# Kernel tuning notes

Hardware: AMD Instinct MI355X
Metric: run time of the kernel (lower is better)

## Reference

```python
import jax, jax.numpy as jnp
import numpy as np

N_NODES = 100000
N_EDGES = 3200000
IN_DIM = 256
OUT_DIM = 256


def setup_inputs() -> dict:
    key = jax.random.key(0)
    k1, k2, k3, k4, k5 = jax.random.split(key, 5)
    x = jax.random.normal(k1, (N_NODES, IN_DIM), dtype=jnp.float32)
    edge_src = jax.random.randint(k2, (N_EDGES,), 0, N_NODES, dtype=jnp.int32)
    edge_dst = jax.random.randint(k3, (N_EDGES,), 0, N_NODES, dtype=jnp.int32)
    # normalized adjacency values (e.g. D^-1/2 A D^-1/2 entries)
    edge_val = jax.random.uniform(k4, (N_EDGES,), dtype=jnp.float32)
    # parameters: uniform(0,1) weight, constant 0.3 bias (matches torch init)
    weight = jax.random.uniform(k5, (IN_DIM, OUT_DIM), dtype=jnp.float32)
    bias = jnp.full((OUT_DIM,), 0.3, dtype=jnp.float32)
    return {"x": x, "edge_src": edge_src, "edge_dst": edge_dst,
            "edge_val": edge_val, "weight": weight, "bias": bias}


def reference(x, edge_src, edge_dst, edge_val, weight, bias):
    # dense feature transform: [N, in] @ [in, out] -> [N, out]
    h = x @ weight
    # sparse adjacency aggregation: out[d] = sum_e val[e] * h[src[e]] for dst[e]==d
    msgs = edge_val[:, None] * h[edge_src]              # [E, out]
    agg = jax.ops.segment_sum(msgs, edge_dst, num_segments=N_NODES)
    return agg + bias
```

## Files before the change

### kernel.cpp

```cpp
#include <hip/hip_runtime.h>

#define FDIM 256
#define BSH 6
#define NBMAX 1600
#define CH 4096
#define NSLOT 7
#define CAPB 2432
#define EPT 10

typedef __attribute__((ext_vector_type(4))) float f32x4;
typedef __attribute__((ext_vector_type(8))) short bf16x8;
typedef unsigned long long u64;

static __device__ __forceinline__ unsigned short f32_to_bf16_rtn(float f) {
    unsigned u = __builtin_bit_cast(unsigned, f);
    u += 0x7FFFu + ((u >> 16) & 1u);
    return (unsigned short)(u >> 16);
}
static __device__ __forceinline__ float bf16_to_f32(unsigned short s) {
    unsigned u = ((unsigned)s) << 16;
    return __builtin_bit_cast(float, u);
}

__global__ __launch_bounds__(256) void convert_bin_kernel(
    const float* __restrict__ x, unsigned short* __restrict__ xh, long n8,
    const float* __restrict__ W, unsigned short* __restrict__ wfrag,
    const int* __restrict__ src, const int* __restrict__ dst, const float* __restrict__ val,
    int* __restrict__ cursors, u64* __restrict__ binned, int n_edges, int nb, int bin_blocks) {
    __shared__ int hist[NBMAX];
    __shared__ int gbase[NBMAX];
    __shared__ int sbase[NBMAX];
    __shared__ int scan_s[256];
    __shared__ u64 stage[CH];
    __shared__ unsigned short bos[CH];

    const int t = threadIdx.x;

    if (blockIdx.x < 32) {
        int tt = blockIdx.x * 256 + t;
        int lane = tt & 63;
        int kt   = (tt >> 6) & 7;
        int nt   = tt >> 9;
        int col  = nt * 16 + (lane & 15);
        int k0   = kt * 32 + 8 * (lane >> 4);
        ushort4 o0, o1;
        o0.x = f32_to_bf16_rtn(W[(k0 + 0) * FDIM + col]);
        o0.y = f32_to_bf16_rtn(W[(k0 + 1) * FDIM + col]);
        o0.z = f32_to_bf16_rtn(W[(k0 + 2) * FDIM + col]);
        o0.w = f32_to_bf16_rtn(W[(k0 + 3) * FDIM + col]);
        o1.x = f32_to_bf16_rtn(W[(k0 + 4) * FDIM + col]);
        o1.y = f32_to_bf16_rtn(W[(k0 + 5) * FDIM + col]);
        o1.z = f32_to_bf16_rtn(W[(k0 + 6) * FDIM + col]);
        o1.w = f32_to_bf16_rtn(W[(k0 + 7) * FDIM + col]);
        ((ushort4*)(wfrag + (size_t)tt * 8))[0] = o0;
        ((ushort4*)(wfrag + (size_t)tt * 8))[1] = o1;
    }

    if (blockIdx.x < bin_blocks) {
        const int chunk0 = blockIdx.x * CH;
        const int m = min(CH, n_edges - chunk0);

        for (int b = t; b < nb; b += 256) hist[b] = 0;
        __syncthreads();
        for (int i = t; i < m; i += 256) atomicAdd(&hist[dst[chunk0 + i] >> BSH], 1);
        __syncthreads();
        for (int b = t; b < nb; b += 256) {
            int c = hist[b];
            gbase[b] = c ? atomicAdd(&cursors[b], c) : 0;
        }
        int loc[NSLOT]; int sum = 0;
        #pragma unroll
        for (int k = 0; k < NSLOT; ++k) {
            int b = t * NSLOT + k;
            int c = (b < nb) ? hist[b] : 0;
            loc[k] = sum; sum += c;
        }
        scan_s[t] = sum;
        __syncthreads();
        #pragma unroll
        for (int off = 1; off < 256; off <<= 1) {
            int u = (t >= off) ? scan_s[t - off] : 0;
            __syncthreads();
            scan_s[t] += u;
            __syncthreads();
        }
        int excl = scan_s[t] - sum;
        #pragma unroll
        for (int k = 0; k < NSLOT; ++k) {
            int b = t * NSLOT + k;
            if (b < nb) sbase[b] = excl + loc[k];
        }
        __syncthreads();
        for (int b = t; b < nb; b += 256) hist[b] = 0;
        __syncthreads();
        for (int i = t; i < m; i += 256) {
            int d = dst[chunk0 + i];
            int b = d >> BSH;
            int p = atomicAdd(&hist[b], 1);
            int slot = sbase[b] + p;
            unsigned w0 = (unsigned)src[chunk0 + i] | ((unsigned)(d & 63) << 17);
            unsigned w1 = __builtin_bit_cast(unsigned, val[chunk0 + i]);
            stage[slot] = (u64)w0 | ((u64)w1 << 32);
            bos[slot]   = (unsigned short)b;
        }
        __syncthreads();
        for (int i = t; i < m; i += 256) {
            int b = bos[i];
            int p = gbase[b] + (i - sbase[b]);
            if (p < CAPB)
                binned[(size_t)b * CAPB + p] = stage[i];
        }
    }

    long i = (long)blockIdx.x * 256 + t;
    long stride = (long)gridDim.x * 256;
    for (long p = i; p < n8; p += stride) {
        const float4* q = (const float4*)(x + p * 8);
        float4 a = q[0], b = q[1];
        ushort4 o0, o1;
        o0.x = f32_to_bf16_rtn(a.x); o0.y = f32_to_bf16_rtn(a.y);
        o0.z = f32_to_bf16_rtn(a.z); o0.w = f32_to_bf16_rtn(a.w);
        o1.x = f32_to_bf16_rtn(b.x); o1.y = f32_to_bf16_rtn(b.y);
        o1.z = f32_to_bf16_rtn(b.z); o1.w = f32_to_bf16_rtn(b.w);
        ((ushort4*)(xh + p * 8))[0] = o0;
        ((ushort4*)(xh + p * 8))[1] = o1;
    }
}

__global__ __launch_bounds__(256) void gather_kernel(
    const unsigned short* __restrict__ xh, const int* __restrict__ cursors,
    const u64* __restrict__ binned,
    float* __restrict__ aggf, unsigned short* __restrict__ aggb, int use_bf16, int n_nodes) {
    __shared__ u64 s2[CAPB];
    __shared__ int cnt[64], startv[64], cur[64];

    const int t = threadIdx.x, b = blockIdx.x;
    const size_t base = (size_t)b * CAPB;
    int m = cursors[b];
    if (m > CAPB) m = CAPB;

    if (t < 64) cnt[t] = 0;
    __syncthreads();
    u64 ereg[EPT];
    int nmine = 0;
    #pragma unroll
    for (int k = 0; k < EPT; ++k) {
        int i = t + k * 256;
        if (i < m) {
            u64 e = binned[base + i];
            ereg[k] = e;
            nmine = k + 1;
            atomicAdd(&cnt[(int)((e >> 17) & 63)], 1);
        }
    }
    __syncthreads();
    if (t < 64) startv[t] = cnt[t];
    __syncthreads();
    #pragma unroll
    for (int off = 1; off < 64; off <<= 1) {
        int u = 0;
        if (t < 64 && t >= off) u = startv[t - off];
        __syncthreads();
        if (t < 64) startv[t] += u;
        __syncthreads();
    }
    if (t < 64) cur[t] = startv[t] - cnt[t];
    __syncthreads();
    #pragma unroll
    for (int k = 0; k < EPT; ++k) {
        if (k < nmine) {
            u64 e = ereg[k];
            int p = atomicAdd(&cur[(int)((e >> 17) & 63)], 1);
            s2[p] = e;
        }
    }
    __syncthreads();

    const int wv = t >> 6, lane = t & 63;
    const int half = lane >> 5, l32 = lane & 31;
    for (int q = 0; q < 16; ++q) {
        const int lo = wv * 16 + q;
        const int node = (b << BSH) + lo;
        const int beg = startv[lo] - cnt[lo];
        const int end = startv[lo];
        float acc[8] = {0.f, 0.f, 0.f, 0.f, 0.f, 0.f, 0.f, 0.f};
        int j = beg;
        for (; j + 16 <= end; j += 16) {
            #pragma unroll
            for (int k = 0; k < 8; ++k) {
                u64 e = s2[j + 2 * k + half];
                float v = __builtin_bit_cast(float, (unsigned)(e >> 32));
                bf16x8 r = *(const bf16x8*)(xh + (((size_t)((unsigned)e & 0x1FFFF)) << 8) + (l32 << 3));
                #pragma unroll
                for (int d = 0; d < 8; ++d)
                    acc[d] += v * bf16_to_f32((unsigned short)r[d]);
            }
        }
        for (; j + 8 <= end; j += 8) {
            #pragma unroll
            for (int k = 0; k < 4; ++k) {
                u64 e = s2[j + 2 * k + half];
                float v = __builtin_bit_cast(float, (unsigned)(e >> 32));
                bf16x8 r = *(const bf16x8*)(xh + (((size_t)((unsigned)e & 0x1FFFF)) << 8) + (l32 << 3));
                #pragma unroll
                for (int d = 0; d < 8; ++d)
                    acc[d] += v * bf16_to_f32((unsigned short)r[d]);
            }
        }
        for (; j < end; j += 2) {
            int idx = j + half;
            u64 e = s2[idx < end ? idx : j];
            float v = (idx < end) ? __builtin_bit_cast(float, (unsigned)(e >> 32)) : 0.f;
            bf16x8 r = *(const bf16x8*)(xh + (((size_t)((unsigned)e & 0x1FFFF)) << 8) + (l32 << 3));
            #pragma unroll
            for (int d = 0; d < 8; ++d)
                acc[d] += v * bf16_to_f32((unsigned short)r[d]);
        }
        #pragma unroll
        for (int d = 0; d < 8; ++d) acc[d] += __shfl_xor(acc[d], 32);
        if (node < n_nodes) {
            float c0 = acc[4 * half + 0], c1 = acc[4 * half + 1];
            float c2 = acc[4 * half + 2], c3 = acc[4 * half + 3];
            if (use_bf16) {
                u64 w = (u64)f32_to_bf16_rtn(c0) | ((u64)f32_to_bf16_rtn(c1) << 16)
                      | ((u64)f32_to_bf16_rtn(c2) << 32) | ((u64)f32_to_bf16_rtn(c3) << 48);
                __builtin_nontemporal_store(w,
                    (u64*)(aggb + ((size_t)node << 8) + (l32 << 3) + (half << 2)));
            } else {
                f32x4 o = {c0, c1, c2, c3};
                __builtin_nontemporal_store(o,
                    (f32x4*)(aggf + ((size_t)node << 8) + (l32 << 3) + (half << 2)));
            }
        }
    }
}

template <bool BF16A>
__global__ __launch_bounds__(256) void gemm_mfma_kernel(
    const void* __restrict__ Araw, const unsigned short* __restrict__ wfrag,
    const float* __restrict__ bias, float* __restrict__ out, int n_rows) {
    int wave = (int)((blockIdx.x * 256u + threadIdx.x) >> 6);
    int lane = threadIdx.x & 63;
    int m0 = wave * 32;
    if (m0 >= n_rows) return;

    f32x4 acc[2][16];
    #pragma unroll
    for (int s = 0; s < 2; ++s)
        #pragma unroll
        for (int i = 0; i < 16; ++i) acc[s][i] = (f32x4)(0.f);

    const int arow0 = m0 + (lane & 15);
    const int arow1 = arow0 + 16;
    const int kbase = 8 * (lane >> 4);

    #pragma unroll
    for (int kt = 0; kt < 8; ++kt) {
        bf16x8 af0, af1;
        if (BF16A) {
            const unsigned short* Ab = (const unsigned short*)Araw;
            af0 = __builtin_nontemporal_load(
                (const bf16x8*)(Ab + (size_t)arow0 * FDIM + kt * 32 + kbase));
            af1 = __builtin_nontemporal_load(
                (const bf16x8*)(Ab + (size_t)arow1 * FDIM + kt * 32 + kbase));
        } else {
            const float* A = (const float*)Araw;
            const f32x4* ap0 = (const f32x4*)(A + (size_t)arow0 * FDIM + kt * 32 + kbase);
            const f32x4* ap1 = (const f32x4*)(A + (size_t)arow1 * FDIM + kt * 32 + kbase);
            f32x4 a0 = __builtin_nontemporal_load(ap0);
            f32x4 a1 = __builtin_nontemporal_load(ap0 + 1);
            f32x4 b0 = __builtin_nontemporal_load(ap1);
            f32x4 b1 = __builtin_nontemporal_load(ap1 + 1);
            #pragma unroll
            for (int j = 0; j < 4; ++j) {
                af0[j]     = (short)f32_to_bf16_rtn(a0[j]);
                af0[j + 4] = (short)f32_to_bf16_rtn(a1[j]);
                af1[j]     = (short)f32_to_bf16_rtn(b0[j]);
                af1[j + 4] = (short)f32_to_bf16_rtn(b1[j]);
            }
        }
        #pragma unroll
        for (int nt = 0; nt < 16; ++nt) {
            bf16x8 bfr = *(const bf16x8*)(wfrag + ((size_t)(nt * 8 + kt) * 64 + lane) * 8);
            acc[0][nt] = __builtin_amdgcn_mfma_f32_16x16x32_bf16(af0, bfr, acc[0][nt], 0, 0, 0);
            acc[1][nt] = __builtin_amdgcn_mfma_f32_16x16x32_bf16(af1, bfr, acc[1][nt], 0, 0, 0);
        }
    }

    const int col = lane & 15;
    #pragma unroll
    for (int s = 0; s < 2; ++s) {
        const int rbase = m0 + s * 16 + 4 * (lane >> 4);
        #pragma unroll
        for (int nt = 0; nt < 16; ++nt) {
            float bv = bias[nt * 16 + col];
            #pragma unroll
            for (int r = 0; r < 4; ++r) {
                int row = rbase + r;
                if (row < n_rows)
                    __builtin_nontemporal_store(acc[s][nt][r] + bv,
                        &out[(size_t)row * FDIM + nt * 16 + col]);
            }
        }
    }
}

extern "C" void kernel_launch(void* const* d_in, const int* in_sizes, int n_in,
                              void* d_out, int out_size, void* d_ws, size_t ws_size,
                              hipStream_t stream) {
    const float* x    = (const float*)d_in[0];
    const int*   src  = (const int*)  d_in[1];
    const int*   dst  = (const int*)  d_in[2];
    const float* val  = (const float*)d_in[3];
    const float* W    = (const float*)d_in[4];
    const float* bias = (const float*)d_in[5];
    float* out = (float*)d_out;

    int n_nodes = in_sizes[0] / FDIM;
    int n_edges = in_sizes[1];
    int nb = (n_nodes + 63) >> BSH;

    int* cursors = (int*)d_ws;
    size_t ioff = ((size_t)nb + 1) & ~(size_t)1;
    u64* binned = (u64*)((int*)d_ws + ioff);
    unsigned short* xh    = (unsigned short*)(binned + (size_t)nb * CAPB);
    unsigned short* wfrag = xh + (size_t)n_nodes * FDIM;
    unsigned short* aggb  = wfrag + 16 * 8 * 64 * 8;

    size_t need = (size_t)((char*)(aggb + (size_t)n_nodes * FDIM) - (char*)d_ws);
    int use_bf16_agg = (ws_size >= need) ? 1 : 0;

    (void)hipMemsetAsync(cursors, 0, (size_t)nb * sizeof(int), stream);

    long n8 = (long)n_nodes * FDIM / 8;
    int bin_blocks = (n_edges + CH - 1) / CH;
    convert_bin_kernel<<<2048, 256, 0, stream>>>(x, xh, n8, W, wfrag,
                                                 src, dst, val, cursors, binned,
                                                 n_edges, nb, bin_blocks);

    gather_kernel<<<nb, 256, 0, stream>>>(xh, cursors, binned,
                                          out, aggb, use_bf16_agg, n_nodes);

    int waves = (n_nodes + 31) / 32;
    int gemm_blocks = (waves + 3) / 4;
    if (use_bf16_agg)
        gemm_mfma_kernel<true><<<gemm_blocks, 256, 0, stream>>>((const void*)aggb, wfrag, bias, out, n_nodes);
    else
        gemm_mfma_kernel<false><<<gemm_blocks, 256, 0, stream>>>((const void*)out, wfrag, bias, out, n_nodes);
}
```

Before: 492.5 us.

## Reorder to transform-then-aggregate, fusing x conversion into GEMM and bias into gather

Computes h = x@W first in a bf16 MFMA GEMM that reads fp32 x directly, stores h as bf16, then gathers over h and adds bias when writing the final output. This removes the separate x-to-bf16 conversion pass and the intermediate aggregated buffer round trip. The cost is that binning no longer overlaps with x conversion, and h is now rounded to bf16 before aggregation.

```diff
diff --git a/kernel.cpp b/kernel.cpp
--- a/kernel.cpp
+++ b/kernel.cpp
@@ -22,11 +22,10 @@
     return __builtin_bit_cast(float, u);
 }
 
-__global__ __launch_bounds__(256) void convert_bin_kernel(
-    const float* __restrict__ x, unsigned short* __restrict__ xh, long n8,
-    const float* __restrict__ W, unsigned short* __restrict__ wfrag,
+__global__ __launch_bounds__(256) void bin_kernel(
     const int* __restrict__ src, const int* __restrict__ dst, const float* __restrict__ val,
-    int* __restrict__ cursors, u64* __restrict__ binned, int n_edges, int nb, int bin_blocks) {
+    int* __restrict__ cursors, u64* __restrict__ binned, int n_edges, int nb,
+    const float* __restrict__ W, unsigned short* __restrict__ wfrag) {
     __shared__ int hist[NBMAX];
     __shared__ int gbase[NBMAX];
     __shared__ int sbase[NBMAX];
@@ -56,81 +55,125 @@
         ((ushort4*)(wfrag + (size_t)tt * 8))[1] = o1;
     }
 
-    if (blockIdx.x < bin_blocks) {
-        const int chunk0 = blockIdx.x * CH;
-        const int m = min(CH, n_edges - chunk0);
-
-        for (int b = t; b < nb; b += 256) hist[b] = 0;
+    const int chunk0 = blockIdx.x * CH;
+    const int m = min(CH, n_edges - chunk0);
+    if (m <= 0) return;
+
+    for (int b = t; b < nb; b += 256) hist[b] = 0;
+    __syncthreads();
+    for (int i = t; i < m; i += 256) atomicAdd(&hist[dst[chunk0 + i] >> BSH], 1);
+    __syncthreads();
+    for (int b = t; b < nb; b += 256) {
+        int c = hist[b];
+        gbase[b] = c ? atomicAdd(&cursors[b], c) : 0;
+    }
+    int loc[NSLOT]; int sum = 0;
+    #pragma unroll
+    for (int k = 0; k < NSLOT; ++k) {
+        int b = t * NSLOT + k;
+        int c = (b < nb) ? hist[b] : 0;
+        loc[k] = sum; sum += c;
+    }
+    scan_s[t] = sum;
+    __syncthreads();
+    #pragma unroll
+    for (int off = 1; off < 256; off <<= 1) {
+        int u = (t >= off) ? scan_s[t - off] : 0;
         __syncthreads();
-        for (int i = t; i < m; i += 256) atomicAdd(&hist[dst[chunk0 + i] >> BSH], 1);
+        scan_s[t] += u;
         __syncthreads();
-        for (int b = t; b < nb; b += 256) {
-            int c = hist[b];
-            gbase[b] = c ? atomicAdd(&cursors[b], c) : 0;
-        }
-        int loc[NSLOT]; int sum = 0;
-        #pragma unroll
-        for (int k = 0; k < NSLOT; ++k) {
-            int b = t * NSLOT + k;
-            int c = (b < nb) ? hist[b] : 0;
-            loc[k] = sum; sum += c;
-        }
-        scan_s[t] = sum;
-        __syncthreads();
-        #pragma unroll
-        for (int off = 1; off < 256; off <<= 1) {
-            int u = (t >= off) ? scan_s[t - off] : 0;
-            __syncthreads();
-            scan_s[t] += u;
-            __syncthreads();
-        }
-        int excl = scan_s[t] - sum;
-        #pragma unroll
-        for (int k = 0; k < NSLOT; ++k) {
-            int b = t * NSLOT + k;
-            if (b < nb) sbase[b] = excl + loc[k];
-        }
-        __syncthreads();
-        for (int b = t; b < nb; b += 256) hist[b] = 0;
-        __syncthreads();
-        for (int i = t; i < m; i += 256) {
-            int d = dst[chunk0 + i];
-            int b = d >> BSH;
-            int p = atomicAdd(&hist[b], 1);
-            int slot = sbase[b] + p;
-            unsigned w0 = (unsigned)src[chunk0 + i] | ((unsigned)(d & 63) << 17);
-            unsigned w1 = __builtin_bit_cast(unsigned, val[chunk0 + i]);
-            stage[slot] = (u64)w0 | ((u64)w1 << 32);
-            bos[slot]   = (unsigned short)b;
-        }
-        __syncthreads();
-        for (int i = t; i < m; i += 256) {
-            int b = bos[i];
-            int p = gbase[b] + (i - sbase[b]);
-            if (p < CAPB)
-                binned[(size_t)b * CAPB + p] = stage[i];
-        }
-    }
-
-    long i = (long)blockIdx.x * 256 + t;
-    long stride = (long)gridDim.x * 256;
-    for (long p = i; p < n8; p += stride) {
-        const float4* q = (const float4*)(x + p * 8);
-        float4 a = q[0], b = q[1];
-        ushort4 o0, o1;
-        o0.x = f32_to_bf16_rtn(a.x); o0.y = f32_to_bf16_rtn(a.y);
-        o0.z = f32_to_bf16_rtn(a.z); o0.w = f32_to_bf16_rtn(a.w);
-        o1.x = f32_to_bf16_rtn(b.x); o1.y = f32_to_bf16_rtn(b.y);
-        o1.z = f32_to_bf16_rtn(b.z); o1.w = f32_to_bf16_rtn(b.w);
-        ((ushort4*)(xh + p * 8))[0] = o0;
-        ((ushort4*)(xh + p * 8))[1] = o1;
+    }
+    int excl = scan_s[t] - sum;
+    #pragma unroll
+    for (int k = 0; k < NSLOT; ++k) {
+        int b = t * NSLOT + k;
+        if (b < nb) sbase[b] = excl + loc[k];
+    }
+    __syncthreads();
+    for (int b = t; b < nb; b += 256) hist[b] = 0;
+    __syncthreads();
+    for (int i = t; i < m; i += 256) {
+        int d = dst[chunk0 + i];
+        int b = d >> BSH;
+        int p = atomicAdd(&hist[b], 1);
+        int slot = sbase[b] + p;
+        unsigned w0 = (unsigned)src[chunk0 + i] | ((unsigned)(d & 63) << 17);
+        unsigned w1 = __builtin_bit_cast(unsigned, val[chunk0 + i]);
+        stage[slot] = (u64)w0 | ((u64)w1 << 32);
+        bos[slot]   = (unsigned short)b;
+    }
+    __syncthreads();
+    for (int i = t; i < m; i += 256) {
+        int b = bos[i];
+        int p = gbase[b] + (i - sbase[b]);
+        if (p < CAPB)
+            binned[(size_t)b * CAPB + p] = stage[i];
+    }
+}
+
+__global__ __launch_bounds__(256) void gemm_h_kernel(
+    const float* __restrict__ x, const unsigned short* __restrict__ wfrag,
+    unsigned short* __restrict__ hb, int n_rows) {
+    int wave = (int)((blockIdx.x * 256u + threadIdx.x) >> 6);
+    int lane = threadIdx.x & 63;
+    int m0 = wave * 32;
+    if (m0 >= n_rows) return;
+
+    f32x4 acc[2][16];
+    #pragma unroll
+    for (int s = 0; s < 2; ++s)
+        #pragma unroll
+        for (int i = 0; i < 16; ++i) acc[s][i] = (f32x4)(0.f);
+
+    const int arow0 = m0 + (lane & 15);
+    const int arow1 = arow0 + 16;
+    const int kbase = 8 * (lane >> 4);
+
+    #pragma unroll
+    for (int kt = 0; kt < 8; ++kt) {
+        const f32x4* ap0 = (const f32x4*)(x + (size_t)arow0 * FDIM + kt * 32 + kbase);
+        const f32x4* ap1 = (const f32x4*)(x + (size_t)arow1 * FDIM + kt * 32 + kbase);
+        f32x4 a0 = __builtin_nontemporal_load(ap0);
+        f32x4 a1 = __builtin_nontemporal_load(ap0 + 1);
+        f32x4 b0 = __builtin_nontemporal_load(ap1);
+        f32x4 b1 = __builtin_nontemporal_load(ap1 + 1);
+        bf16x8 af0, af1;
+        #pragma unroll
+        for (int j = 0; j < 4; ++j) {
+            af0[j]     = (short)f32_to_bf16_rtn(a0[j]);
+            af0[j + 4] = (short)f32_to_bf16_rtn(a1[j]);
+            af1[j]     = (short)f32_to_bf16_rtn(b0[j]);
+            af1[j + 4] = (short)f32_to_bf16_rtn(b1[j]);
+        }
+        #pragma unroll
+        for (int nt = 0; nt < 16; ++nt) {
+            bf16x8 bfr = *(const bf16x8*)(wfrag + ((size_t)(nt * 8 + kt) * 64 + lane) * 8);
+            acc[0][nt] = __builtin_amdgcn_mfma_f32_16x16x32_bf16(af0, bfr, acc[0][nt], 0, 0, 0);
+            acc[1][nt] = __builtin_amdgcn_mfma_f32_16x16x32_bf16(af1, bfr, acc[1][nt], 0, 0, 0);
+        }
+    }
+
+    const int col = lane & 15;
+    #pragma unroll
+    for (int s = 0; s < 2; ++s) {
+        const int rbase = m0 + s * 16 + 4 * (lane >> 4);
+        #pragma unroll
+        for (int nt = 0; nt < 16; ++nt) {
+            #pragma unroll
+            for (int r = 0; r < 4; ++r) {
+                int row = rbase + r;
+                if (row < n_rows)
+                    __builtin_nontemporal_store(f32_to_bf16_rtn(acc[s][nt][r]),
+                        &hb[(size_t)row * FDIM + nt * 16 + col]);
+            }
+        }
     }
 }
 
 __global__ __launch_bounds__(256) void gather_kernel(
-    const unsigned short* __restrict__ xh, const int* __restrict__ cursors,
-    const u64* __restrict__ binned,
-    float* __restrict__ aggf, unsigned short* __restrict__ aggb, int use_bf16, int n_nodes) {
+    const unsigned short* __restrict__ hb, const int* __restrict__ cursors,
+    const u64* __restrict__ binned, const float* __restrict__ bias,
+    float* __restrict__ out, int n_nodes) {
     __shared__ u64 s2[CAPB];
     __shared__ int cnt[64], startv[64], cur[64];
 
@@ -178,6 +221,9 @@
 
     const int wv = t >> 6, lane = t & 63;
     const int half = lane >> 5, l32 = lane & 31;
+    const int dbase = (l32 << 3) + (half << 2);
+    const f32x4 bv = *(const f32x4*)(bias + dbase);
+
     for (int q = 0; q < 16; ++q) {
         const int lo = wv * 16 + q;
         const int node = (b << BSH) + lo;
@@ -190,7 +236,7 @@
             for (int k = 0; k < 8; ++k) {
                 u64 e = s2[j + 2 * k + half];
                 float v = __builtin_bit_cast(float, (unsigned)(e >> 32));
-                bf16x8 r = *(const bf16x8*)(xh + (((size_t)((unsigned)e & 0x1FFFF)) << 8) + (l32 << 3));
+                bf16x8 r = *(const bf16x8*)(hb + (((size_t)((unsigned)e & 0x1FFFF)) << 8) + (l32 << 3));
                 #pragma unroll
                 for (int d = 0; d < 8; ++d)
                     acc[d] += v * bf16_to_f32((unsigned short)r[d]);
@@ -201,7 +247,7 @@
             for (int k = 0; k < 4; ++k) {
                 u64 e = s2[j + 2 * k + half];
                 float v = __builtin_bit_cast(float, (unsigned)(e >> 32));
-                bf16x8 r = *(const bf16x8*)(xh + (((size_t)((unsigned)e & 0x1FFFF)) << 8) + (l32 << 3));
+                bf16x8 r = *(const bf16x8*)(hb + (((size_t)((unsigned)e & 0x1FFFF)) << 8) + (l32 << 3));
                 #pragma unroll
                 for (int d = 0; d < 8; ++d)
                     acc[d] += v * bf16_to_f32((unsigned short)r[d]);
@@ -211,7 +257,7 @@
             int idx = j + half;
             u64 e = s2[idx < end ? idx : j];
             float v = (idx < end) ? __builtin_bit_cast(float, (unsigned)(e >> 32)) : 0.f;
-            bf16x8 r = *(const bf16x8*)(xh + (((size_t)((unsigned)e & 0x1FFFF)) << 8) + (l32 << 3));
+            bf16x8 r = *(const bf16x8*)(hb + (((size_t)((unsigned)e & 0x1FFFF)) << 8) + (l32 << 3));
             #pragma unroll
             for (int d = 0; d < 8; ++d)
                 acc[d] += v * bf16_to_f32((unsigned short)r[d]);
@@ -219,88 +265,9 @@
         #pragma unroll
         for (int d = 0; d < 8; ++d) acc[d] += __shfl_xor(acc[d], 32);
         if (node < n_nodes) {
-            float c0 = acc[4 * half + 0], c1 = acc[4 * half + 1];
-            float c2 = acc[4 * half + 2], c3 = acc[4 * half + 3];
-            if (use_bf16) {
-                u64 w = (u64)f32_to_bf16_rtn(c0) | ((u64)f32_to_bf16_rtn(c1) << 16)
-                      | ((u64)f32_to_bf16_rtn(c2) << 32) | ((u64)f32_to_bf16_rtn(c3) << 48);
-                __builtin_nontemporal_store(w,
-                    (u64*)(aggb + ((size_t)node << 8) + (l32 << 3) + (half << 2)));
-            } else {
-                f32x4 o = {c0, c1, c2, c3};
-                __builtin_nontemporal_store(o,
-                    (f32x4*)(aggf + ((size_t)node << 8) + (l32 << 3) + (half << 2)));
-            }
-        }
-    }
-}
-
-template <bool BF16A>
-__global__ __launch_bounds__(256) void gemm_mfma_kernel(
-    const void* __restrict__ Araw, const unsigned short* __restrict__ wfrag,
-    const float* __restrict__ bias, float* __restrict__ out, int n_rows) {
-    int wave = (int)((blockIdx.x * 256u + threadIdx.x) >> 6);
-    int lane = threadIdx.x & 63;
-    int m0 = wave * 32;
-    if (m0 >= n_rows) return;
-
-    f32x4 acc[2][16];
-    #pragma unroll
-    for (int s = 0; s < 2; ++s)
-        #pragma unroll
-        for (int i = 0; i < 16; ++i) acc[s][i] = (f32x4)(0.f);
-
-    const int arow0 = m0 + (lane & 15);
-    const int arow1 = arow0 + 16;
-    const int kbase = 8 * (lane >> 4);
-
-    #pragma unroll
-    for (int kt = 0; kt < 8; ++kt) {
-        bf16x8 af0, af1;
-        if (BF16A) {
-            const unsigned short* Ab = (const unsigned short*)Araw;
-            af0 = __builtin_nontemporal_load(
-                (const bf16x8*)(Ab + (size_t)arow0 * FDIM + kt * 32 + kbase));
-            af1 = __builtin_nontemporal_load(
-                (const bf16x8*)(Ab + (size_t)arow1 * FDIM + kt * 32 + kbase));
-        } else {
-            const float* A = (const float*)Araw;
-            const f32x4* ap0 = (const f32x4*)(A + (size_t)arow0 * FDIM + kt * 32 + kbase);
-            const f32x4* ap1 = (const f32x4*)(A + (size_t)arow1 * FDIM + kt * 32 + kbase);
-            f32x4 a0 = __builtin_nontemporal_load(ap0);
-            f32x4 a1 = __builtin_nontemporal_load(ap0 + 1);
-            f32x4 b0 = __builtin_nontemporal_load(ap1);
-            f32x4 b1 = __builtin_nontemporal_load(ap1 + 1);
-            #pragma unroll
-            for (int j = 0; j < 4; ++j) {
-                af0[j]     = (short)f32_to_bf16_rtn(a0[j]);
-                af0[j + 4] = (short)f32_to_bf16_rtn(a1[j]);
-                af1[j]     = (short)f32_to_bf16_rtn(b0[j]);
-                af1[j + 4] = (short)f32_to_bf16_rtn(b1[j]);
-            }
-        }
-        #pragma unroll
-        for (int nt = 0; nt < 16; ++nt) {
-            bf16x8 bfr = *(const bf16x8*)(wfrag + ((size_t)(nt * 8 + kt) * 64 + lane) * 8);
-            acc[0][nt] = __builtin_amdgcn_mfma_f32_16x16x32_bf16(af0, bfr, acc[0][nt], 0, 0, 0);
-            acc[1][nt] = __builtin_amdgcn_mfma_f32_16x16x32_bf16(af1, bfr, acc[1][nt], 0, 0, 0);
-        }
-    }
-
-    const int col = lane & 15;
-    #pragma unroll
-    for (int s = 0; s < 2; ++s) {
-        const int rbase = m0 + s * 16 + 4 * (lane >> 4);
-        #pragma unroll
-        for (int nt = 0; nt < 16; ++nt) {
-            float bv = bias[nt * 16 + col];
-            #pragma unroll
-            for (int r = 0; r < 4; ++r) {
-                int row = rbase + r;
-                if (row < n_rows)
-                    __builtin_nontemporal_store(acc[s][nt][r] + bv,
-                        &out[(size_t)row * FDIM + nt * 16 + col]);
-            }
+            f32x4 o = {acc[4 * half + 0] + bv[0], acc[4 * half + 1] + bv[1],
+                       acc[4 * half + 2] + bv[2], acc[4 * half + 3] + bv[3]};
+            __builtin_nontemporal_store(o, (f32x4*)(out + ((size_t)node << 8) + dbase));
         }
     }
 }
@@ -323,28 +290,18 @@
     int* cursors = (int*)d_ws;
     size_t ioff = ((size_t)nb + 1) & ~(size_t)1;
     u64* binned = (u64*)((int*)d_ws + ioff);
-    unsigned short* xh    = (unsigned short*)(binned + (size_t)nb * CAPB);
-    unsigned short* wfrag = xh + (size_t)n_nodes * FDIM;
-    unsigned short* aggb  = wfrag + 16 * 8 * 64 * 8;
-
-    size_t need = (size_t)((char*)(aggb + (size_t)n_nodes * FDIM) - (char*)d_ws);
-    int use_bf16_agg = (ws_size >= need) ? 1 : 0;
+    unsigned short* hb    = (unsigned short*)(binned + (size_t)nb * CAPB);
+    unsigned short* wfrag = hb + (size_t)n_nodes * FDIM;
 
     (void)hipMemsetAsync(cursors, 0, (size_t)nb * sizeof(int), stream);
 
-    long n8 = (long)n_nodes * FDIM / 8;
     int bin_blocks = (n_edges + CH - 1) / CH;
-    convert_bin_kernel<<<2048, 256, 0, stream>>>(x, xh, n8, W, wfrag,
-                                                 src, dst, val, cursors, binned,
-                                                 n_edges, nb, bin_blocks);
-
-    gather_kernel<<<nb, 256, 0, stream>>>(xh, cursors, binned,
-                                          out, aggb, use_bf16_agg, n_nodes);
+    bin_kernel<<<bin_blocks, 256, 0, stream>>>(src, dst, val, cursors, binned, n_edges, nb,
+                                               W, wfrag);
 
     int waves = (n_nodes + 31) / 32;
     int gemm_blocks = (waves + 3) / 4;
-    if (use_bf16_agg)
-        gemm_mfma_kernel<true><<<gemm_blocks, 256, 0, stream>>>((const void*)aggb, wfrag, bias, out, n_nodes);
-    else
-        gemm_mfma_kernel<false><<<gemm_blocks, 256, 0, stream>>>((const void*)out, wfrag, bias, out, n_nodes);
-}
+    gemm_h_kernel<<<gemm_blocks, 256, 0, stream>>>(x, wfrag, hb, n_nodes);
+
+    gather_kernel<<<nb, 256, 0, stream>>>(hb, cursors, binned, bias, out, n_nodes);
+}
```

New measurement: 493.4 us. About the same (+0.2%).
